# Kernel tuning notes

Hardware: AMD Instinct MI355X
Metric: run time of the kernel (lower is better)

## Reference

```python
import jax, jax.numpy as jnp
import numpy as np

WORLD_SIZE = 8
M = 4096
N = 4096
K_LOCAL = 1024  # full K = WORLD_SIZE * K_LOCAL = 8192


def setup_inputs() -> dict:
    key = jax.random.key(0)
    k1, k2 = jax.random.split(key)
    # Per-rank activation shard [R, M, K_local] and weight shard [R, N, K_local]
    inp = jax.random.normal(k1, (WORLD_SIZE, M, K_LOCAL), dtype=jnp.float32) * 0.02
    w = jax.random.normal(k2, (WORLD_SIZE, N, K_LOCAL), dtype=jnp.float32) * 0.02
    return {"input": inp, "weight": w}


def reference(input, weight):
    # Each rank r computes a partial GEMM: input[r] @ weight[r].T -> [M, N].
    # Reduce(-scatter) sums partials over ranks; the single einsum contracts
    # both the rank axis (the all-reduce part) and K_local (the GEMM part).
    full = jnp.einsum("rmk,rnk->mn", input, weight)  # [M, N]
    R = input.shape[0]
    # Scatter: rank r receives rows [r*M/R : (r+1)*M/R] -> stacked [R, M/R, N]
    return full.reshape(R, full.shape[0] // R, full.shape[1])
```

## Files before the change

### kernel.cpp

```cpp
#include <hip/hip_runtime.h>
#include <cstdint>
#include <cstddef>


#define M_DIM 4096
#define N_DIM 4096
#define K_DIM 8192
#define K_LOCAL 1024
#define RANKS 8

typedef __bf16 bf16x8 __attribute__((ext_vector_type(8)));
typedef float f32x4 __attribute__((ext_vector_type(4)));

__device__ __forceinline__ unsigned short f2bf(float f) {
    unsigned int u = __float_as_uint(f);
    unsigned int r = (u + 0x7fffu + ((u >> 16) & 1u)) >> 16;
    return (unsigned short)r;
}

__global__ __launch_bounds__(256) void convert_cast(
    const float* __restrict__ srcA, unsigned short* __restrict__ dstA,
    const float* __restrict__ srcB, unsigned short* __restrict__ dstB,
    int blocks_per_tensor) {
    const float* src = srcA;
    unsigned short* dst = dstA;
    int b = blockIdx.x;
    if (b >= blocks_per_tensor) { b -= blocks_per_tensor; src = srcB; dst = dstB; }
    size_t base = (size_t)b * 4096 + threadIdx.x * 4;
#pragma unroll
    for (int i = 0; i < 4; ++i) {
        size_t e = base + i * 1024;
        f32x4 v = __builtin_nontemporal_load((const f32x4*)(src + e));
        ushort4 o;
        o.x = f2bf(v.x); o.y = f2bf(v.y); o.z = f2bf(v.z); o.w = f2bf(v.w);
        *(ushort4*)(dst + e) = o;
    }
}

__device__ __forceinline__ void gll16(const unsigned short* g, unsigned short* l) {
    __builtin_amdgcn_global_load_lds(
        (const __attribute__((address_space(1))) void*)g,
        (__attribute__((address_space(3))) void*)l,
        16, 0, 0);
}

__device__ __forceinline__ int k_off(int t) {
    return ((t >> 4) << 22) | ((t & 15) << 6);
}

#define VM6 asm volatile("s_waitcnt vmcnt(6)" ::: "memory")
#define VM0 asm volatile("s_waitcnt vmcnt(0)" ::: "memory")
#define VMNONE ((void)0)
#define LGKM0 asm volatile("s_waitcnt lgkmcnt(0)" ::: "memory")
#define LGKM8 asm volatile("s_waitcnt lgkmcnt(8)" ::: "memory")

#define STAGE_A(TOFF, HALF, PBUF) { \
    _Pragma("unroll") for (int j_ = 0; j_ < 2; ++j_) \
        gll16(A + (size_t)((TOFF) + (HALF) * 131072 + thrA[j_]), \
              smem + (PBUF) * 16384 + (HALF) * 8192 + ldsOff[j_]); }

#define STAGE_B(TOFF, HALF, PBUF) { \
    _Pragma("unroll") for (int j_ = 0; j_ < 2; ++j_) \
        gll16(B + (size_t)((TOFF) + (HALF) * 131072 + thrB[j_]), \
              smem + 32768 + (PBUF) * 16384 + (HALF) * 8192 + ldsOff[j_]); }

#define READ_A(DST, BASE, MOFF) { \
    _Pragma("unroll") for (int ks_ = 0; ks_ < 2; ++ks_) \
        _Pragma("unroll") for (int mm_ = 0; mm_ < 4; ++mm_) \
            DST[ks_][mm_] = *(const bf16x8*)&(BASE)[(((MOFF) + mm_) * 16 + l15) * 64 + (ks_ ? swz1 : swz0)]; }

#define READ_B(DST, BASE, NJ0) { \
    _Pragma("unroll") for (int ks_ = 0; ks_ < 2; ++ks_) \
        _Pragma("unroll") for (int nn_ = 0; nn_ < 2; ++nn_) \
            DST[ks_][nn_] = *(const bf16x8*)&(BASE)[(bRowBase + ((NJ0) + nn_) * 16 + l15) * 64 + (ks_ ? swz1 : swz0)]; }

#define QUAD(AF, BF, MI0, NJ0) { \
    __builtin_amdgcn_s_setprio(1); \
    _Pragma("unroll") for (int ks_ = 0; ks_ < 2; ++ks_) \
        _Pragma("unroll") for (int mm_ = 0; mm_ < 4; ++mm_) \
            _Pragma("unroll") for (int nn_ = 0; nn_ < 2; ++nn_) \
                acc[(MI0) + mm_][(NJ0) + nn_] = __builtin_amdgcn_mfma_f32_16x16x32_bf16( \
                    AF[ks_][mm_], BF[ks_][nn_], acc[(MI0) + mm_][(NJ0) + nn_], 0, 0, 0); \
    __builtin_amdgcn_s_setprio(0); }

#define KTILE16(PBUF, KT, SB1, SA, SB0, VMOP) { \
    const int t1off_ = k_off((KT) + 1); \
    const int t2off_ = k_off((KT) + 2); \
    unsigned short* aC_ = smem + (PBUF) * 16384 + wmIdx * 8192; \
    unsigned short* bC_ = smem + 32768 + (PBUF) * 16384 + bHalfSel * 8192; \
     \
    READ_A(aLo, aC_, 0) \
    READ_B(bLoF, bC_, 0) \
    if (SB1) { STAGE_B(t1off_, 1, (PBUF) ^ 1) } \
    LGKM8; \
    __builtin_amdgcn_s_barrier(); \
    LGKM0; \
    QUAD(aLo, bLoF, 0, 0) \
    __builtin_amdgcn_s_barrier(); \
     \
    READ_A(aHi, aC_, 4) \
    __builtin_amdgcn_s_barrier(); \
    LGKM0; \
    QUAD(aHi, bLoF, 4, 0) \
    __builtin_amdgcn_s_barrier(); \
     \
    READ_B(bHiF, bC_, 2) \
    if (SA) { STAGE_A(t2off_, 0, (PBUF)) } \
    __builtin_amdgcn_s_barrier(); \
    LGKM0; \
    QUAD(aLo, bHiF, 0, 2) \
    __builtin_amdgcn_s_barrier(); \
     \
    if (SA) { STAGE_A(t2off_, 1, (PBUF)) } \
    if (SB0) { STAGE_B(t2off_, 0, (PBUF)) } \
    __builtin_amdgcn_s_barrier(); \
    LGKM0; \
    QUAD(aHi, bHiF, 4, 2) \
    VMOP; \
    __builtin_amdgcn_s_barrier(); \
}

__global__ __launch_bounds__(512, 2) void gemm_bf16_8ph(
    const unsigned short* __restrict__ A,
    const unsigned short* __restrict__ B,
    float* __restrict__ C) {
    extern __shared__ unsigned short smem[];

    const int tid = threadIdx.x;
    const int lane = tid & 63;
    const int wave = tid >> 6;
    const int wmIdx = wave >> 2;
    const int wn = wave & 3;
    const int l15 = lane & 15;
    const int l4 = lane >> 4;
    const int bHalfSel = wn >> 1;
    const int bRowBase = (wn & 1) * 64;

    const int bid = blockIdx.x;
    const int xcd = bid & 7;
    const int idx = bid >> 3;
    const int tm = (xcd >> 2) * 8 + (idx >> 2);
    const int tn = (xcd & 3) * 4 + (idx & 3);
    const int bm0 = tm * 256;
    const int bn0 = tn * 256;

    int thrA[2], thrB[2], ldsOff[2];
#pragma unroll
    for (int j = 0; j < 2; ++j) {
        int cc = j * 512 + tid;
        int row = cc >> 3;
        int col = ((cc & 7) ^ (row & 7)) * 8;
        thrA[j] = (bm0 + row) * K_LOCAL + col;
        thrB[j] = (bn0 + row) * K_LOCAL + col;
        ldsOff[j] = cc * 8;
    }

    const int swz0 = ((0 + l4) ^ (l15 & 7)) * 8;
    const int swz1 = ((4 + l4) ^ (l15 & 7)) * 8;

    bf16x8 aLo[2][4], aHi[2][4], bLoF[2][2], bHiF[2][2];
    f32x4 acc[8][4] = {};

    STAGE_A(0, 0, 0)
    STAGE_A(0, 1, 0)
    STAGE_B(0, 0, 0)
    STAGE_B(0, 1, 0)
    STAGE_A(64, 0, 1)
    STAGE_A(64, 1, 1)
    STAGE_B(64, 0, 1)
    VM6;
    __builtin_amdgcn_s_barrier();

#pragma unroll 1
    for (int kt = 0; kt < 126; kt += 2) {
        KTILE16(0, kt, 1, 1, 1, VM6)
        KTILE16(1, kt + 1, 1, 1, 1, VM6)
    }
    KTILE16(0, 126, 1, 0, 0, VM0)
    KTILE16(1, 127, 0, 0, 0, VMNONE)

#pragma unroll
    for (int mi = 0; mi < 8; ++mi) {
        int row0 = bm0 + wmIdx * 128 + mi * 16 + l4 * 4;
#pragma unroll
        for (int nj = 0; nj < 4; ++nj) {
            int col = bn0 + wn * 64 + nj * 16 + l15;
#pragma unroll
            for (int r = 0; r < 4; ++r)
                C[(size_t)(row0 + r) * N_DIM + col] = acc[mi][nj][r];
        }
    }
}

__global__ __launch_bounds__(256) void gemm_bf16_128(
    const unsigned short* __restrict__ A,
    const unsigned short* __restrict__ B,
    float* __restrict__ C) {
    __shared__ __align__(16) unsigned short As[128 * 64];
    __shared__ __align__(16) unsigned short Bs[128 * 64];

    const int tid = threadIdx.x;
    const int lane = tid & 63;
    const int wave = tid >> 6;
    const int wm = (wave >> 1) * 64;
    const int wnn = (wave & 1) * 64;
    const int l15 = lane & 15;
    const int l4 = lane >> 4;

    const int bid = blockIdx.x;
    const int xcd = bid & 7;
    const int q = bid >> 3;
    const int st = (q >> 2) * 8 + xcd;
    const int pos = q & 3;
    const int bm0 = ((st >> 4) * 2 + (pos >> 1)) * 128;
    const int bn0 = ((st & 15) * 2 + (pos & 1)) * 128;

    const unsigned short* ga[4];
    const unsigned short* gb[4];
    int lo[4];
#pragma unroll
    for (int p = 0; p < 4; ++p) {
        int cc = p * 256 + tid;
        int row = cc >> 3;
        int cpos = cc & 7;
        int col = (cpos ^ (row & 7)) * 8;
        ga[p] = A + (size_t)(bm0 + row) * K_LOCAL + col;
        gb[p] = B + (size_t)(bn0 + row) * K_LOCAL + col;
        lo[p] = cc * 8;
    }

    const int swz0 = ((l4 + 0) ^ (l15 & 7)) * 8;
    const int swz1 = ((l4 + 4) ^ (l15 & 7)) * 8;
    const int a_row = (wm + l15) * 64;
    const int b_row = (wnn + l15) * 64;

    f32x4 acc[4][4] = {};

    for (int r = 0; r < RANKS; ++r) {
        const size_t roff = (size_t)r * (M_DIM * (size_t)K_LOCAL);
        for (int kl = 0; kl < K_LOCAL; kl += 64) {
#pragma unroll
            for (int p = 0; p < 4; ++p) {
                gll16(ga[p] + roff + kl, &As[lo[p]]);
                gll16(gb[p] + roff + kl, &Bs[lo[p]]);
            }
            __syncthreads();
#pragma unroll
            for (int ks = 0; ks < 2; ++ks) {
                const int swz = ks ? swz1 : swz0;
                bf16x8 af[4], bfr[4];
#pragma unroll
                for (int i = 0; i < 4; ++i)
                    af[i] = *(const bf16x8*)&As[a_row + i * 16 * 64 + swz];
#pragma unroll
                for (int j = 0; j < 4; ++j)
                    bfr[j] = *(const bf16x8*)&Bs[b_row + j * 16 * 64 + swz];
#pragma unroll
                for (int i = 0; i < 4; ++i)
#pragma unroll
                    for (int j = 0; j < 4; ++j)
                        acc[i][j] = __builtin_amdgcn_mfma_f32_16x16x32_bf16(
                            af[i], bfr[j], acc[i][j], 0, 0, 0);
            }
            __syncthreads();
        }
    }

#pragma unroll
    for (int i = 0; i < 4; ++i) {
        int row0 = bm0 + wm + i * 16 + l4 * 4;
#pragma unroll
        for (int j = 0; j < 4; ++j) {
            int col = bn0 + wnn + j * 16 + l15;
#pragma unroll
            for (int r = 0; r < 4; ++r)
                C[(size_t)(row0 + r) * N_DIM + col] = acc[i][j][r];
        }
    }
}

__global__ void gemm_naive(const float* __restrict__ A, const float* __restrict__ B,
                           float* __restrict__ C) {
    __shared__ float As[16][17];
    __shared__ float Bs[16][17];
    int tx = threadIdx.x, ty = threadIdx.y;
    int m = blockIdx.y * 16 + ty;
    int n0 = blockIdx.x * 16;
    float accv = 0.f;
    for (int kt = 0; kt < K_DIM; kt += 16) {
        int r = kt >> 10;
        int k = (kt & 1023) + tx;
        As[ty][tx] = A[((size_t)r * M_DIM + m) * K_LOCAL + k];
        Bs[ty][tx] = B[((size_t)r * N_DIM + (n0 + ty)) * K_LOCAL + k];
        __syncthreads();
#pragma unroll
        for (int kk = 0; kk < 16; ++kk) accv += As[ty][kk] * Bs[tx][kk];
        __syncthreads();
    }
    C[(size_t)m * N_DIM + n0 + tx] = accv;
}

extern "C" void kernel_launch(void* const* d_in, const int* in_sizes, int n_in,
                              void* d_out, int out_size, void* d_ws, size_t ws_size,
                              hipStream_t stream) {
    const float* inp = (const float*)d_in[0];
    const float* wgt = (const float*)d_in[1];
    float* out = (float*)d_out;

    const size_t elems = (size_t)M_DIM * K_DIM;
    const size_t need = 2 * elems * sizeof(unsigned short);

    if (ws_size >= need) {
        unsigned short* Abf = (unsigned short*)d_ws;
        unsigned short* Bbf = Abf + elems;
        const int bpt = (int)(elems / 4096);
        convert_cast<<<bpt * 2, 256, 0, stream>>>(inp, Abf, wgt, Bbf, bpt);

        static int dynOK = -1;
        if (dynOK < 0) {
            dynOK = (hipFuncSetAttribute((const void*)gemm_bf16_8ph,
                                         hipFuncAttributeMaxDynamicSharedMemorySize,
                                         131072) == hipSuccess)
                        ? 1
                        : 0;
        }
        if (dynOK) {
            gemm_bf16_8ph<<<256, 512, 131072, stream>>>(Abf, Bbf, out);
        } else {
            gemm_bf16_128<<<1024, 256, 0, stream>>>(Abf, Bbf, out);
        }
    } else {
        dim3 grid(N_DIM / 16, M_DIM / 16);
        dim3 block(16, 16);
        gemm_naive<<<grid, block, 0, stream>>>(inp, wgt, out);
    }
}
```

Measured before the change: 278.9 us.

## Restructure GEMM k-tile pipeline to prefetch next-tile fragments and drop LDS waits

Reorganizes the 8-phase bf16 GEMM main loop so each phase issues LDS reads for the next quadrant while MFMAs run on already-loaded fragments. The next k-tile's low A/B fragments are read at the end of the current tile, and the explicit lgkmcnt waits plus the extra barriers per phase are removed, leaving one barrier per phase. Global-to-LDS staging is regrouped and vmcnt thresholds are adjusted. This aims to hide LDS latency and cut barrier count, at the risk of more register pressure and relying on compiler-inserted waits for correctness.

```diff
diff --git a/kernel.cpp b/kernel.cpp
--- a/kernel.cpp
+++ b/kernel.cpp
@@ -48,11 +48,11 @@
     return ((t >> 4) << 22) | ((t & 15) << 6);
 }
 
-#define VM6 asm volatile("s_waitcnt vmcnt(6)" ::: "memory")
+#define VM8 asm volatile("s_waitcnt vmcnt(8)" ::: "memory")
+#define VM2 asm volatile("s_waitcnt vmcnt(2)" ::: "memory")
 #define VM0 asm volatile("s_waitcnt vmcnt(0)" ::: "memory")
 #define VMNONE ((void)0)
-#define LGKM0 asm volatile("s_waitcnt lgkmcnt(0)" ::: "memory")
-#define LGKM8 asm volatile("s_waitcnt lgkmcnt(8)" ::: "memory")
+#define BAR __builtin_amdgcn_s_barrier();
 
 #define STAGE_A(TOFF, HALF, PBUF) { \
     _Pragma("unroll") for (int j_ = 0; j_ < 2; ++j_) \
@@ -83,41 +83,30 @@
                     AF[ks_][mm_], BF[ks_][nn_], acc[(MI0) + mm_][(NJ0) + nn_], 0, 0, 0); \
     __builtin_amdgcn_s_setprio(0); }
 
-#define KTILE16(PBUF, KT, SB1, SA, SB0, VMOP) { \
-    const int t1off_ = k_off((KT) + 1); \
+#define KTILE(PBUF, KT, S3, S4, SR, VMOP) { \
     const int t2off_ = k_off((KT) + 2); \
     unsigned short* aC_ = smem + (PBUF) * 16384 + wmIdx * 8192; \
     unsigned short* bC_ = smem + 32768 + (PBUF) * 16384 + bHalfSel * 8192; \
-     \
-    READ_A(aLo, aC_, 0) \
-    READ_B(bLoF, bC_, 0) \
-    if (SB1) { STAGE_B(t1off_, 1, (PBUF) ^ 1) } \
-    LGKM8; \
-    __builtin_amdgcn_s_barrier(); \
-    LGKM0; \
-    QUAD(aLo, bLoF, 0, 0) \
-    __builtin_amdgcn_s_barrier(); \
+    unsigned short* aN_ = smem + ((PBUF) ^ 1) * 16384 + wmIdx * 8192; \
+    unsigned short* bN_ = smem + 32768 + ((PBUF) ^ 1) * 16384 + bHalfSel * 8192; \
      \
     READ_A(aHi, aC_, 4) \
-    __builtin_amdgcn_s_barrier(); \
-    LGKM0; \
-    QUAD(aHi, bLoF, 4, 0) \
-    __builtin_amdgcn_s_barrier(); \
+    QUAD(aLo, bLo, 0, 0) \
+    BAR \
      \
-    READ_B(bHiF, bC_, 2) \
-    if (SA) { STAGE_A(t2off_, 0, (PBUF)) } \
-    __builtin_amdgcn_s_barrier(); \
-    LGKM0; \
-    QUAD(aLo, bHiF, 0, 2) \
-    __builtin_amdgcn_s_barrier(); \
+    READ_B(bHi, bC_, 2) \
+    QUAD(aHi, bLo, 4, 0) \
+    BAR \
      \
-    if (SA) { STAGE_A(t2off_, 1, (PBUF)) } \
-    if (SB0) { STAGE_B(t2off_, 0, (PBUF)) } \
-    __builtin_amdgcn_s_barrier(); \
-    LGKM0; \
-    QUAD(aHi, bHiF, 4, 2) \
+    if (S3) { STAGE_A(t2off_, 0, (PBUF)) } \
+    QUAD(aLo, bHi, 0, 2) \
     VMOP; \
-    __builtin_amdgcn_s_barrier(); \
+    BAR \
+     \
+    if (SR) { READ_A(aLo, aN_, 0) READ_B(bLo, bN_, 0) } \
+    if (S4) { STAGE_A(t2off_, 1, (PBUF)) STAGE_B(t2off_, 0, (PBUF)) STAGE_B(t2off_, 1, (PBUF)) } \
+    QUAD(aHi, bHi, 4, 2) \
+    BAR \
 }
 
 __global__ __launch_bounds__(512, 2) void gemm_bf16_8ph(
@@ -158,7 +147,7 @@
     const int swz0 = ((0 + l4) ^ (l15 & 7)) * 8;
     const int swz1 = ((4 + l4) ^ (l15 & 7)) * 8;
 
-    bf16x8 aLo[2][4], aHi[2][4], bLoF[2][2], bHiF[2][2];
+    bf16x8 aLo[2][4], aHi[2][4], bLo[2][2], bHi[2][2];
     f32x4 acc[8][4] = {};
 
     STAGE_A(0, 0, 0)
@@ -168,16 +157,23 @@
     STAGE_A(64, 0, 1)
     STAGE_A(64, 1, 1)
     STAGE_B(64, 0, 1)
-    VM6;
-    __builtin_amdgcn_s_barrier();
+    STAGE_B(64, 1, 1)
+    VM8;
+    BAR
+    {
+        unsigned short* a0_ = smem + wmIdx * 8192;
+        unsigned short* b0_ = smem + 32768 + bHalfSel * 8192;
+        READ_A(aLo, a0_, 0)
+        READ_B(bLo, b0_, 0)
+    }
 
 #pragma unroll 1
     for (int kt = 0; kt < 126; kt += 2) {
-        KTILE16(0, kt, 1, 1, 1, VM6)
-        KTILE16(1, kt + 1, 1, 1, 1, VM6)
-    }
-    KTILE16(0, 126, 1, 0, 0, VM0)
-    KTILE16(1, 127, 0, 0, 0, VMNONE)
+        KTILE(0, kt, 1, 1, 1, VM2)
+        KTILE(1, kt + 1, 1, 1, 1, VM2)
+    }
+    KTILE(0, 126, 0, 0, 1, VM0)
+    KTILE(1, 127, 0, 0, 0, VMNONE)
 
 #pragma unroll
     for (int mi = 0; mi < 8; ++mi) {
```

Result: faster. 266.1 us (-4.6%).
